# Kernel tuning notes

Hardware: AMD Instinct MI355X
Metric: run time of the kernel (lower is better)

## Reference

```python
import jax, jax.numpy as jnp
import numpy as np

D_MODEL = 1024
H = 16
D_HEAD = D_MODEL // H
MASK_VAL = -1e30


def setup_inputs() -> dict:
    key = jax.random.key(0)
    ks = jax.random.split(key, 10)
    B, S = 2, 2048
    scale = 1.0 / np.sqrt(D_MODEL)
    return {
        "query": jax.random.normal(ks[0], (B, S, D_MODEL), jnp.float32),
        "key": jax.random.normal(ks[1], (B, S, D_MODEL), jnp.float32),
        "value": jax.random.normal(ks[2], (B, S, D_MODEL), jnp.float32),
        "mask": jax.random.randint(ks[3], (B, S, S), 0, 2) > 0,
        "Wq": jax.random.normal(ks[4], (D_MODEL, D_MODEL), jnp.float32) * scale,
        "bq": jnp.zeros((D_MODEL,), jnp.float32),
        "Wk": jax.random.normal(ks[5], (D_MODEL, D_MODEL), jnp.float32) * scale,
        "bk": jnp.zeros((D_MODEL,), jnp.float32),
        "Wv": jax.random.normal(ks[6], (D_MODEL, D_MODEL), jnp.float32) * scale,
        "bv": jnp.zeros((D_MODEL,), jnp.float32),
    }


def _split_heads(x, B, S):
    # [B,S,D] -> [B,H,S,Dh]
    return x.reshape(B, S, H, D_HEAD).transpose(0, 2, 1, 3)


def reference(query, key, value, mask, Wq, bq, Wk, bk, Wv, bv):
    B, S, _ = query.shape
    q = _split_heads(query @ Wq.T + bq, B, S)
    k = _split_heads(key @ Wk.T + bk, B, S)
    v = _split_heads(value @ Wv.T + bv, B, S)
    # scale by sqrt of per-head dim (query.size(-1) after split)
    q = q / jnp.sqrt(jnp.asarray(D_HEAD, q.dtype))
    scores = jnp.einsum("bhqd,bhkd->bhqk", q, k)
    scores = jnp.where(mask[:, None, :, :], MASK_VAL, scores)
    attn = jax.nn.softmax(scores, axis=-1)
    out = jnp.einsum("bhqk,bhkd->bhqd", attn, v)
    return out.transpose(0, 2, 1, 3).reshape(B, S, D_MODEL)
```

## Files before the change

### kernel.cpp

```cpp
#include <hip/hip_runtime.h>
#include <hip/hip_bf16.h>

#define D_MODEL 1024
#define NH 16
#define DH 64
#define S_LEN 2048
#define BATCH 2
#define NEG_BIG -3e38f
#define QSCALE (0.125f * 1.44269504088896f)

#define KV_HSTRIDE (S_LEN * DH)
#define WS_V_OFF   (NH * KV_HSTRIDE)
#define KVB_WORDS  (2 * NH * KV_HSTRIDE)
#define MB_WORDS   ((S_LEN / 64) * S_LEN)
#define KTILE 128
#define NT (S_LEN / KTILE)
#define X_ELEMS (BATCH * S_LEN * D_MODEL)
#define W_ELEMS (D_MODEL * D_MODEL)
#define KSTR 88

typedef __attribute__((ext_vector_type(8))) short bf16x8;
typedef __attribute__((ext_vector_type(4))) float f32x4;

static __device__ inline unsigned short f2bf(float f) {
    union { float f; unsigned u; } v; v.f = f;
    unsigned r = v.u + 0x7fffu + ((v.u >> 16) & 1u);
    return (unsigned short)(r >> 16);
}
static __device__ inline unsigned cvt2(float a, float b) {
    union { __hip_bfloat162 h2; unsigned u; } cv;
    cv.h2 = __float22bfloat162_rn(make_float2(a, b));
    return cv.u;
}
static __device__ inline bf16x8 pack8(f32x4 a, f32x4 b) {
    union { bf16x8 v; unsigned u[4]; } r;
    r.u[0] = cvt2(a[0], a[1]); r.u[1] = cvt2(a[2], a[3]);
    r.u[2] = cvt2(b[0], b[1]); r.u[3] = cvt2(b[2], b[3]);
    return r.v;
}
static __device__ inline bf16x8 cvt8(const float* __restrict__ p) {
    return pack8(*(const f32x4*)p, *(const f32x4*)(p + 4));
}
static __device__ inline float exp2_fast(float x) {
#if __has_builtin(__builtin_amdgcn_exp2f)
    return __builtin_amdgcn_exp2f(x);
#else
    return exp2f(x);
#endif
}
static __device__ inline void gload_lds16(const unsigned short* __restrict__ g,
                                          unsigned short* l, int lane) {
#if __has_builtin(__builtin_amdgcn_global_load_lds)
    __builtin_amdgcn_global_load_lds(
        (const __attribute__((address_space(1))) void*)g,
        (__attribute__((address_space(3))) void*)l, 16, 0, 0);
#else
    *(bf16x8*)((char*)l + lane * 16) = *(const bf16x8*)g;
#endif
}
static __device__ inline int vperm(int s) {
    return (s & ~31) | ((s & 12) << 1) | ((s & 16) >> 2) | (s & 3);
}

__global__ __launch_bounds__(256) void cvt_kernel(
    const float* __restrict__ q, const float* __restrict__ k,
    const float* __restrict__ v,
    const float* __restrict__ Wq, const float* __restrict__ Wk,
    const float* __restrict__ Wv,
    unsigned short* __restrict__ xb, unsigned short* __restrict__ wb)
{
    const int by = blockIdx.y;
    const float* src;
    unsigned short* dst;
    int t;
    if (blockIdx.x < 1024) {
        src = by == 0 ? q : (by == 1 ? k : v);
        dst = xb + (size_t)by * X_ELEMS;
        t = blockIdx.x * 256 + threadIdx.x;
    } else {
        src = by == 0 ? Wq : (by == 1 ? Wk : Wv);
        dst = wb + (size_t)by * W_ELEMS;
        t = (blockIdx.x - 1024) * 256 + threadIdx.x;
    }
    const size_t o = (size_t)t * 16;
    *(bf16x8*)&dst[o]     = cvt8(src + o);
    *(bf16x8*)&dst[o + 8] = cvt8(src + o + 8);
}

__global__ __launch_bounds__(256) void pack_mask_kernel(
    const int* __restrict__ mask, unsigned long long* __restrict__ mbits,
    int b_base)
{
    const int w    = blockIdx.x * 4 + (threadIdx.x >> 6);
    const int lane = threadIdx.x & 63;
    const int b    = b_base + (w >> 16);
    const int rem  = w & 65535;
    const int kt   = rem >> 11;
    const int s    = rem & 2047;
    const int v = mask[((size_t)b * S_LEN + s) * S_LEN + kt * 64 + lane];
    const unsigned long long bits = __ballot(v != 0);
    if (lane == 0) mbits[w] = bits;
}

__global__ __launch_bounds__(256) void proj_v2_kernel(
    const unsigned short* __restrict__ xb, const unsigned short* __restrict__ wb,
    const float* __restrict__ bq, const float* __restrict__ bk,
    const float* __restrict__ bv,
    float* __restrict__ q_out, unsigned short* __restrict__ ws)
{
    const int bx = blockIdx.x;
    const int by = blockIdx.y;
    const int z  = by >> 3;
    const int c0 = (by & 7) * 128;

    const unsigned short* A  = xb + (size_t)z * X_ELEMS;
    const unsigned short* Bw = wb + (size_t)z * W_ELEMS;
    const float* bias = z == 0 ? bq : (z == 1 ? bk : bv);

    const int tid  = threadIdx.x;
    const int wave = tid >> 6;
    const int lane = tid & 63;
    const int quad = lane >> 4;
    const int l16  = lane & 15;
    const int m0   = (wave & 1) * 64;
    const int n0   = (wave >> 1) * 64;

    __shared__ __align__(16) unsigned short As[128 * 32];
    __shared__ __align__(16) unsigned short Bs[128 * 32];

    const int r_lo = wave * 16 + (lane >> 2);
    const int r_hi = (wave + 4) * 16 + (lane >> 2);
    const int segu = (lane & 3) * 8;
    const int row0 = bx * 128;

    f32x4 acc[4][4] = {};

    for (int kk = 0; kk < D_MODEL; kk += 32) {
        gload_lds16(A  + (size_t)(row0 + r_lo) * D_MODEL + kk + segu, &As[wave * 512], lane);
        gload_lds16(A  + (size_t)(row0 + r_hi) * D_MODEL + kk + segu, &As[(wave + 4) * 512], lane);
        gload_lds16(Bw + (size_t)(c0 + r_lo) * D_MODEL + kk + segu, &Bs[wave * 512], lane);
        gload_lds16(Bw + (size_t)(c0 + r_hi) * D_MODEL + kk + segu, &Bs[(wave + 4) * 512], lane);
        __syncthreads();

        bf16x8 af[4], bfr[4];
#pragma unroll
        for (int i = 0; i < 4; ++i)
            af[i] = *(const bf16x8*)&As[(m0 + i * 16 + l16) * 32 + quad * 8];
#pragma unroll
        for (int j = 0; j < 4; ++j)
            bfr[j] = *(const bf16x8*)&Bs[(n0 + j * 16 + l16) * 32 + quad * 8];
#pragma unroll
        for (int i = 0; i < 4; ++i)
#pragma unroll
            for (int j = 0; j < 4; ++j)
                acc[i][j] = __builtin_amdgcn_mfma_f32_16x16x32_bf16(
                    af[i], bfr[j], acc[i][j], 0, 0, 0);
        __syncthreads();
    }

#pragma unroll
    for (int j = 0; j < 4; ++j) {
        const int cl  = c0 + n0 + j * 16 + l16;
        const float bval = bias[cl];
        const int h  = cl >> 6;
        const int dh = cl & 63;
#pragma unroll
        for (int i = 0; i < 4; ++i) {
#pragma unroll
            for (int r = 0; r < 4; ++r) {
                const int row = row0 + m0 + i * 16 + quad * 4 + r;
                const float v = acc[i][j][r] + bval;
                if (z == 0) {
                    q_out[(size_t)row * D_MODEL + cl] = v * QSCALE;
                } else {
                    unsigned short* slab = ws + (size_t)(row >> 11) * KVB_WORDS;
                    const int s = row & 2047;
                    if (z == 1)
                        slab[(size_t)h * KV_HSTRIDE + s * DH + dh] = f2bf(v);
                    else
                        slab[WS_V_OFF + (size_t)h * KV_HSTRIDE + dh * S_LEN + vperm(s)] = f2bf(v);
                }
            }
        }
    }
}

__global__ __launch_bounds__(256) void proj_fb_kernel(
    const float* __restrict__ q_in, const float* __restrict__ k_in,
    const float* __restrict__ v_in,
    const float* __restrict__ Wq, const float* __restrict__ bq,
    const float* __restrict__ Wk, const float* __restrict__ bk,
    const float* __restrict__ Wv, const float* __restrict__ bv,
    float* __restrict__ q_out, unsigned short* __restrict__ ws, int b_base)
{
    const int bx = blockIdx.x;
    const int by = blockIdx.y;
    const int z  = by >> 3;
    const int c0 = (by & 7) * 128;

    const float* x    = z == 0 ? q_in : (z == 1 ? k_in : v_in);
    const float* W    = z == 0 ? Wq   : (z == 1 ? Wk   : Wv);
    const float* bias = z == 0 ? bq   : (z == 1 ? bk   : bv);

    const int tid  = threadIdx.x;
    const int wave = tid >> 6;
    const int lane = tid & 63;
    const int quad = lane >> 4;
    const int l16  = lane & 15;
    const int m0   = (wave & 1) * 64;
    const int n0   = (wave >> 1) * 64;

    __shared__ __align__(16) unsigned short As[128][40];
    __shared__ __align__(16) unsigned short Bs[128][40];

    const int srow = tid >> 1;
    const int kcol = (tid & 1) * 16;
    const int row0 = b_base * S_LEN + bx * 128;
    const float* ag = x + (size_t)(row0 + srow) * D_MODEL + kcol;
    const float* bg = W + (size_t)(c0 + srow) * D_MODEL + kcol;

    f32x4 acc[4][4] = {};

    for (int kk = 0; kk < D_MODEL; kk += 32) {
        {
            f32x4 a0 = *(const f32x4*)(ag + kk);
            f32x4 a1 = *(const f32x4*)(ag + kk + 4);
            f32x4 a2 = *(const f32x4*)(ag + kk + 8);
            f32x4 a3 = *(const f32x4*)(ag + kk + 12);
            f32x4 b0 = *(const f32x4*)(bg + kk);
            f32x4 b1 = *(const f32x4*)(bg + kk + 4);
            f32x4 b2 = *(const f32x4*)(bg + kk + 8);
            f32x4 b3 = *(const f32x4*)(bg + kk + 12);
            *(bf16x8*)&As[srow][kcol]     = pack8(a0, a1);
            *(bf16x8*)&As[srow][kcol + 8] = pack8(a2, a3);
            *(bf16x8*)&Bs[srow][kcol]     = pack8(b0, b1);
            *(bf16x8*)&Bs[srow][kcol + 8] = pack8(b2, b3);
        }
        __syncthreads();

        bf16x8 af[4], bfr[4];
#pragma unroll
        for (int i = 0; i < 4; ++i)
            af[i] = *(const bf16x8*)&As[m0 + i * 16 + l16][quad * 8];
#pragma unroll
        for (int j = 0; j < 4; ++j)
            bfr[j] = *(const bf16x8*)&Bs[n0 + j * 16 + l16][quad * 8];
#pragma unroll
        for (int i = 0; i < 4; ++i)
#pragma unroll
            for (int j = 0; j < 4; ++j)
                acc[i][j] = __builtin_amdgcn_mfma_f32_16x16x32_bf16(
                    af[i], bfr[j], acc[i][j], 0, 0, 0);
        __syncthreads();
    }

#pragma unroll
    for (int j = 0; j < 4; ++j) {
        const int cl  = c0 + n0 + j * 16 + l16;
        const float bval = bias[cl];
        const int h  = cl >> 6;
        const int dh = cl & 63;
#pragma unroll
        for (int i = 0; i < 4; ++i) {
#pragma unroll
            for (int r = 0; r < 4; ++r) {
                const int row = row0 + m0 + i * 16 + quad * 4 + r;
                const float v = acc[i][j][r] + bval;
                if (z == 0) {
                    q_out[(size_t)row * D_MODEL + cl] = v * QSCALE;
                } else {
                    const int b_rel = (row >> 11) - b_base;
                    const int s     = row & 2047;
                    unsigned short* slab = ws + (size_t)b_rel * KVB_WORDS;
                    if (z == 1)
                        slab[(size_t)h * KV_HSTRIDE + s * DH + dh] = f2bf(v);
                    else
                        slab[WS_V_OFF + (size_t)h * KV_HSTRIDE + dh * S_LEN + vperm(s)] = f2bf(v);
                }
            }
        }
    }
}

__global__ __launch_bounds__(256) void attn_kernel(
    const unsigned short* __restrict__ ws,
    const unsigned long long* __restrict__ mbits,
    const int* __restrict__ mask,
    float* __restrict__ out, int b_base, int use_bits)
{
    const int h     = blockIdx.x;
    const int qtile = blockIdx.y;
    const int bz    = blockIdx.z;
    const int b0    = b_base + bz;

    const unsigned short* K  = ws + (size_t)bz * KVB_WORDS + (size_t)h * KV_HSTRIDE;
    const unsigned short* Vg = K + WS_V_OFF;
    const unsigned long long* mb = mbits + (size_t)bz * MB_WORDS;

    const int tid  = threadIdx.x;
    const int wave = tid >> 6;
    const int lane = tid & 63;
    const int quad = lane >> 4;
    const int l16  = lane & 15;
    const int q0   = qtile * 64;

    __shared__ __align__(16) unsigned short Vt[64][136];
    __shared__ __align__(16) unsigned short Kt[128 * KSTR];

    bf16x8 aq0, aq1;
    {
        const float* qrow =
            out + (size_t)(b0 * S_LEN + q0 + wave * 16 + l16) * D_MODEL + h * DH;
        aq0 = cvt8(qrow + quad * 8);
        aq1 = cvt8(qrow + 32 + quad * 8);
    }

    const int qg = q0 + wave * 16 + l16;
    float l_lane = 0.f;
    f32x4 o_acc[4] = {};

    const int krow = tid >> 1, kc = (tid & 1) * 32;
    const int vrow = tid >> 2, vc = (tid & 3) * 32;
    bf16x8 kr[4], vr[4];
    {
        const unsigned short* kp = K + (size_t)krow * DH + kc;
        const unsigned short* vp = Vg + (size_t)vrow * S_LEN + vc;
#pragma unroll
        for (int i = 0; i < 4; ++i) {
            kr[i] = *(const bf16x8*)(kp + 8 * i);
            vr[i] = *(const bf16x8*)(vp + 8 * i);
        }
    }

    for (int kt = 0; kt < NT; ++kt) {
#pragma unroll
        for (int i = 0; i < 4; ++i) {
            *(bf16x8*)&Kt[krow * KSTR + kc + 8 * i] = kr[i];
            *(bf16x8*)&Vt[vrow][vc + 8 * i]         = vr[i];
        }
        __syncthreads();

        if (kt + 1 < NT) {
            const unsigned short* kp = K + (size_t)((kt + 1) * KTILE + krow) * DH + kc;
            const unsigned short* vp = Vg + (size_t)vrow * S_LEN + (kt + 1) * KTILE + vc;
#pragma unroll
            for (int i = 0; i < 4; ++i) {
                kr[i] = *(const bf16x8*)(kp + 8 * i);
                vr[i] = *(const bf16x8*)(vp + 8 * i);
            }
        }

        unsigned long long wm0 = 0ull, wm1 = 0ull;
        if (use_bits) {
            wm0 = mb[(size_t)(2 * kt) * S_LEN + qg] >> (quad * 4);
            wm1 = mb[(size_t)(2 * kt + 1) * S_LEN + qg] >> (quad * 4);
        }

        f32x4 s[8];
#pragma unroll
        for (int blk = 0; blk < 8; ++blk) {
            const unsigned short* kb = &Kt[(blk * 16 + l16) * KSTR];
            bf16x8 k0 = *(const bf16x8*)&kb[quad * 8];
            bf16x8 k1 = *(const bf16x8*)&kb[32 + quad * 8];
            s[blk] = (f32x4){0.f, 0.f, 0.f, 0.f};
            s[blk] = __builtin_amdgcn_mfma_f32_16x16x32_bf16(k0, aq0, s[blk], 0, 0, 0);
            s[blk] = __builtin_amdgcn_mfma_f32_16x16x32_bf16(k1, aq1, s[blk], 0, 0, 0);
        }

#pragma unroll
        for (int blk = 0; blk < 8; ++blk) {
            const unsigned long long w = (blk < 4) ? wm0 : wm1;
            const int sh = (blk & 3) * 16;
#pragma unroll
            for (int r = 0; r < 4; ++r) {
                bool masked;
                if (use_bits) {
                    masked = (w >> (sh + r)) & 1ull;
                } else {
                    const int kg = kt * KTILE + blk * 16 + quad * 4 + r;
                    masked = mask[((size_t)(b0 * S_LEN) + qg) * S_LEN + kg] != 0;
                }
                const float p = masked ? 0.0f : exp2_fast(s[blk][r]);
                s[blk][r] = p;
                l_lane += p;
            }
        }

        bf16x8 af[4];
#pragma unroll
        for (int c = 0; c < 4; ++c) {
            union { bf16x8 v; unsigned u[4]; } pk;
            pk.u[0] = cvt2(s[2 * c][0],     s[2 * c][1]);
            pk.u[1] = cvt2(s[2 * c][2],     s[2 * c][3]);
            pk.u[2] = cvt2(s[2 * c + 1][0], s[2 * c + 1][1]);
            pk.u[3] = cvt2(s[2 * c + 1][2], s[2 * c + 1][3]);
            af[c] = pk.v;
        }

#pragma unroll
        for (int d = 0; d < 4; ++d) {
#pragma unroll
            for (int c = 0; c < 4; ++c) {
                bf16x8 bv = *(const bf16x8*)&Vt[d * 16 + l16][c * 32 + quad * 8];
                o_acc[d] = __builtin_amdgcn_mfma_f32_16x16x32_bf16(af[c], bv, o_acc[d], 0, 0, 0);
            }
        }
        __syncthreads();
    }

    l_lane += __shfl_xor(l_lane, 16, 64);
    l_lane += __shfl_xor(l_lane, 32, 64);

#pragma unroll
    for (int r = 0; r < 4; ++r) {
        const float lsum = __shfl(l_lane, quad * 4 + r, 64);
        const float inv  = 1.0f / fmaxf(lsum, 1e-30f);
        const int qgr = q0 + wave * 16 + quad * 4 + r;
#pragma unroll
        for (int d = 0; d < 4; ++d)
            out[((size_t)(b0 * S_LEN) + qgr) * D_MODEL + h * DH + d * 16 + l16] =
                o_acc[d][r] * inv;
    }
}

extern "C" void kernel_launch(void* const* d_in, const int* in_sizes, int n_in,
                              void* d_out, int out_size, void* d_ws, size_t ws_size,
                              hipStream_t stream) {
    const float* query = (const float*)d_in[0];
    const float* key   = (const float*)d_in[1];
    const float* value = (const float*)d_in[2];
    const int*   mask  = (const int*)d_in[3];
    const float* Wq    = (const float*)d_in[4];
    const float* bq    = (const float*)d_in[5];
    const float* Wk    = (const float*)d_in[6];
    const float* bk    = (const float*)d_in[7];
    const float* Wv    = (const float*)d_in[8];
    const float* bv    = (const float*)d_in[9];

    unsigned short* ws   = (unsigned short*)d_ws;
    float*          outp = (float*)d_out;

    const size_t KV_BYTES = (size_t)KVB_WORDS * 2;
    const size_t MB_BYTES = (size_t)MB_WORDS * 8;
    const size_t XB_BYTES = (size_t)3 * X_ELEMS * 2;
    const size_t WB_BYTES = (size_t)3 * W_ELEMS * 2;
    const size_t base2    = 2 * KV_BYTES + 2 * MB_BYTES;

    if (ws_size >= base2 + XB_BYTES + WB_BYTES) {
        unsigned long long* mbits = (unsigned long long*)(ws + 2 * KVB_WORDS);
        unsigned short* xb = ws + base2 / 2;
        unsigned short* wb = xb + (size_t)3 * X_ELEMS;
        cvt_kernel<<<dim3(1280, 3), 256, 0, stream>>>(
            query, key, value, Wq, Wk, Wv, xb, wb);
        proj_v2_kernel<<<dim3(32, 24), 256, 0, stream>>>(
            xb, wb, bq, bk, bv, outp, ws);
        pack_mask_kernel<<<dim3(2 * MB_WORDS / 4), 256, 0, stream>>>(mask, mbits, 0);
        attn_kernel<<<dim3(NH, S_LEN / 64, 2), 256, 0, stream>>>(
            ws, mbits, mask, outp, 0, 1);
    } else if (ws_size >= base2) {
        unsigned long long* mbits = (unsigned long long*)(ws + 2 * KVB_WORDS);
        proj_fb_kernel<<<dim3(32, 24), 256, 0, stream>>>(
            query, key, value, Wq, bq, Wk, bk, Wv, bv, outp, ws, 0);
        pack_mask_kernel<<<dim3(2 * MB_WORDS / 4), 256, 0, stream>>>(mask, mbits, 0);
        attn_kernel<<<dim3(NH, S_LEN / 64, 2), 256, 0, stream>>>(
            ws, mbits, mask, outp, 0, 1);
    } else if (ws_size >= KV_BYTES + MB_BYTES) {
        unsigned long long* mbits = (unsigned long long*)(ws + KVB_WORDS);
        for (int b0 = 0; b0 < BATCH; ++b0) {
            proj_fb_kernel<<<dim3(16, 24), 256, 0, stream>>>(
                query, key, value, Wq, bq, Wk, bk, Wv, bv, outp, ws, b0);
            pack_mask_kernel<<<dim3(MB_WORDS / 4), 256, 0, stream>>>(mask, mbits, b0);
            attn_kernel<<<dim3(NH, S_LEN / 64, 1), 256, 0, stream>>>(
                ws, mbits, mask, outp, b0, 1);
        }
    } else {
        for (int b0 = 0; b0 < BATCH; ++b0) {
            proj_fb_kernel<<<dim3(16, 24), 256, 0, stream>>>(
                query, key, value, Wq, bq, Wk, bk, Wv, bv, outp, ws, b0);
            attn_kernel<<<dim3(NH, S_LEN / 64, 1), 256, 0, stream>>>(
                ws, (const unsigned long long*)ws, mask, outp, b0, 0);
        }
    }
}
```

Before: 274.4 us.

## Fuse mask packing into convert kernel, double K-step in projection, MFMA row sums

The f32-to-bf16 convert kernel and the mask bit-packing kernel now run as one flattened launch, which removes a kernel launch and lets the two memory-bound passes overlap. The projection GEMM loads two 32-wide K chunks per barrier pair, so it synchronises half as often at the cost of twice the LDS. The attention kernel computes softmax row sums with an extra MFMA against a ones vector, replacing per-element scalar adds and the final cross-lane shuffles. Because the sum now uses bf16-rounded probabilities, the normaliser matches the P·V product more closely but differs slightly from before.

```diff
diff --git a/kernel.cpp b/kernel.cpp
--- a/kernel.cpp
+++ b/kernel.cpp
@@ -6,7 +6,6 @@
 #define DH 64
 #define S_LEN 2048
 #define BATCH 2
-#define NEG_BIG -3e38f
 #define QSCALE (0.125f * 1.44269504088896f)
 
 #define KV_HSTRIDE (S_LEN * DH)
@@ -62,29 +61,50 @@
     return (s & ~31) | ((s & 12) << 1) | ((s & 16) >> 2) | (s & 3);
 }
 
-__global__ __launch_bounds__(256) void cvt_kernel(
+__global__ __launch_bounds__(256) void cvtpack_kernel(
     const float* __restrict__ q, const float* __restrict__ k,
     const float* __restrict__ v,
     const float* __restrict__ Wq, const float* __restrict__ Wk,
     const float* __restrict__ Wv,
-    unsigned short* __restrict__ xb, unsigned short* __restrict__ wb)
+    unsigned short* __restrict__ xb, unsigned short* __restrict__ wb,
+    const int* __restrict__ mask, unsigned long long* __restrict__ mbits)
 {
-    const int by = blockIdx.y;
-    const float* src;
-    unsigned short* dst;
-    int t;
-    if (blockIdx.x < 1024) {
-        src = by == 0 ? q : (by == 1 ? k : v);
-        dst = xb + (size_t)by * X_ELEMS;
-        t = blockIdx.x * 256 + threadIdx.x;
+    const int bid = blockIdx.x;
+    if (bid < 3840) {
+        const int z = bid / 1280;
+        const int r = bid - z * 1280;
+        const float* src;
+        unsigned short* dst;
+        int t;
+        if (r < 1024) {
+            src = z == 0 ? q : (z == 1 ? k : v);
+            dst = xb + (size_t)z * X_ELEMS;
+            t = r * 256 + threadIdx.x;
+        } else {
+            src = z == 0 ? Wq : (z == 1 ? Wk : Wv);
+            dst = wb + (size_t)z * W_ELEMS;
+            t = (r - 1024) * 256 + threadIdx.x;
+        }
+        const size_t o = (size_t)t * 16;
+        *(bf16x8*)&dst[o]     = cvt8(src + o);
+        *(bf16x8*)&dst[o + 8] = cvt8(src + o + 8);
     } else {
-        src = by == 0 ? Wq : (by == 1 ? Wk : Wv);
-        dst = wb + (size_t)by * W_ELEMS;
-        t = (blockIdx.x - 1024) * 256 + threadIdx.x;
-    }
-    const size_t o = (size_t)t * 16;
-    *(bf16x8*)&dst[o]     = cvt8(src + o);
-    *(bf16x8*)&dst[o + 8] = cvt8(src + o + 8);
+        const int pb   = bid - 3840;
+        const int wave = threadIdx.x >> 6;
+        const int lane = threadIdx.x & 63;
+        const int w0   = pb * 16 + wave * 4;
+#pragma unroll
+        for (int j = 0; j < 4; ++j) {
+            const int w   = w0 + j;
+            const int b   = w >> 16;
+            const int rem = w & 65535;
+            const int kt  = rem >> 11;
+            const int s   = rem & 2047;
+            const int vm  = mask[((size_t)b * S_LEN + s) * S_LEN + kt * 64 + lane];
+            const unsigned long long bits = __ballot(vm != 0);
+            if (lane == 0) mbits[w] = bits;
+        }
+    }
 }
 
 __global__ __launch_bounds__(256) void pack_mask_kernel(
@@ -125,8 +145,8 @@
     const int m0   = (wave & 1) * 64;
     const int n0   = (wave >> 1) * 64;
 
-    __shared__ __align__(16) unsigned short As[128 * 32];
-    __shared__ __align__(16) unsigned short Bs[128 * 32];
+    __shared__ __align__(16) unsigned short As[2][128 * 32];
+    __shared__ __align__(16) unsigned short Bs[2][128 * 32];
 
     const int r_lo = wave * 16 + (lane >> 2);
     const int r_hi = (wave + 4) * 16 + (lane >> 2);
@@ -135,26 +155,33 @@
 
     f32x4 acc[4][4] = {};
 
-    for (int kk = 0; kk < D_MODEL; kk += 32) {
-        gload_lds16(A  + (size_t)(row0 + r_lo) * D_MODEL + kk + segu, &As[wave * 512], lane);
-        gload_lds16(A  + (size_t)(row0 + r_hi) * D_MODEL + kk + segu, &As[(wave + 4) * 512], lane);
-        gload_lds16(Bw + (size_t)(c0 + r_lo) * D_MODEL + kk + segu, &Bs[wave * 512], lane);
-        gload_lds16(Bw + (size_t)(c0 + r_hi) * D_MODEL + kk + segu, &Bs[(wave + 4) * 512], lane);
+    for (int kk = 0; kk < D_MODEL; kk += 64) {
+#pragma unroll
+        for (int c = 0; c < 2; ++c) {
+            const int ko = kk + c * 32 + segu;
+            gload_lds16(A  + (size_t)(row0 + r_lo) * D_MODEL + ko, &As[c][wave * 512], lane);
+            gload_lds16(A  + (size_t)(row0 + r_hi) * D_MODEL + ko, &As[c][(wave + 4) * 512], lane);
+            gload_lds16(Bw + (size_t)(c0 + r_lo) * D_MODEL + ko, &Bs[c][wave * 512], lane);
+            gload_lds16(Bw + (size_t)(c0 + r_hi) * D_MODEL + ko, &Bs[c][(wave + 4) * 512], lane);
+        }
         __syncthreads();
 
-        bf16x8 af[4], bfr[4];
-#pragma unroll
-        for (int i = 0; i < 4; ++i)
-            af[i] = *(const bf16x8*)&As[(m0 + i * 16 + l16) * 32 + quad * 8];
-#pragma unroll
-        for (int j = 0; j < 4; ++j)
-            bfr[j] = *(const bf16x8*)&Bs[(n0 + j * 16 + l16) * 32 + quad * 8];
-#pragma unroll
-        for (int i = 0; i < 4; ++i)
+#pragma unroll
+        for (int c = 0; c < 2; ++c) {
+            bf16x8 af[4], bfr[4];
+#pragma unroll
+            for (int i = 0; i < 4; ++i)
+                af[i] = *(const bf16x8*)&As[c][(m0 + i * 16 + l16) * 32 + quad * 8];
 #pragma unroll
             for (int j = 0; j < 4; ++j)
-                acc[i][j] = __builtin_amdgcn_mfma_f32_16x16x32_bf16(
-                    af[i], bfr[j], acc[i][j], 0, 0, 0);
+                bfr[j] = *(const bf16x8*)&Bs[c][(n0 + j * 16 + l16) * 32 + quad * 8];
+#pragma unroll
+            for (int i = 0; i < 4; ++i)
+#pragma unroll
+                for (int j = 0; j < 4; ++j)
+                    acc[i][j] = __builtin_amdgcn_mfma_f32_16x16x32_bf16(
+                        af[i], bfr[j], acc[i][j], 0, 0, 0);
+        }
         __syncthreads();
     }
 
@@ -315,8 +342,16 @@
         aq1 = cvt8(qrow + 32 + quad * 8);
     }
 
+    bf16x8 ones;
+    {
+        union { bf16x8 v; unsigned short u[8]; } o;
+#pragma unroll
+        for (int i = 0; i < 8; ++i) o.u[i] = 0x3F80;
+        ones = o.v;
+    }
+
     const int qg = q0 + wave * 16 + l16;
-    float l_lane = 0.f;
+    f32x4 l_acc = {0.f, 0.f, 0.f, 0.f};
     f32x4 o_acc[4] = {};
 
     const int krow = tid >> 1, kc = (tid & 1) * 32;
@@ -380,9 +415,7 @@
                     const int kg = kt * KTILE + blk * 16 + quad * 4 + r;
                     masked = mask[((size_t)(b0 * S_LEN) + qg) * S_LEN + kg] != 0;
                 }
-                const float p = masked ? 0.0f : exp2_fast(s[blk][r]);
-                s[blk][r] = p;
-                l_lane += p;
+                s[blk][r] = masked ? 0.0f : exp2_fast(s[blk][r]);
             }
         }
 
@@ -398,6 +431,10 @@
         }
 
 #pragma unroll
+        for (int c = 0; c < 4; ++c)
+            l_acc = __builtin_amdgcn_mfma_f32_16x16x32_bf16(af[c], ones, l_acc, 0, 0, 0);
+
+#pragma unroll
         for (int d = 0; d < 4; ++d) {
 #pragma unroll
             for (int c = 0; c < 4; ++c) {
@@ -408,13 +445,9 @@
         __syncthreads();
     }
 
-    l_lane += __shfl_xor(l_lane, 16, 64);
-    l_lane += __shfl_xor(l_lane, 32, 64);
-
 #pragma unroll
     for (int r = 0; r < 4; ++r) {
-        const float lsum = __shfl(l_lane, quad * 4 + r, 64);
-        const float inv  = 1.0f / fmaxf(lsum, 1e-30f);
+        const float inv = 1.0f / fmaxf(l_acc[r], 1e-30f);
         const int qgr = q0 + wave * 16 + quad * 4 + r;
 #pragma unroll
         for (int d = 0; d < 4; ++d)
@@ -450,11 +483,10 @@
         unsigned long long* mbits = (unsigned long long*)(ws + 2 * KVB_WORDS);
         unsigned short* xb = ws + base2 / 2;
         unsigned short* wb = xb + (size_t)3 * X_ELEMS;
-        cvt_kernel<<<dim3(1280, 3), 256, 0, stream>>>(
-            query, key, value, Wq, Wk, Wv, xb, wb);
+        cvtpack_kernel<<<dim3(3840 + 8192), 256, 0, stream>>>(
+            query, key, value, Wq, Wk, Wv, xb, wb, mask, mbits);
         proj_v2_kernel<<<dim3(32, 24), 256, 0, stream>>>(
             xb, wb, bq, bk, bv, outp, ws);
-        pack_mask_kernel<<<dim3(2 * MB_WORDS / 4), 256, 0, stream>>>(mask, mbits, 0);
         attn_kernel<<<dim3(NH, S_LEN / 64, 2), 256, 0, stream>>>(
             ws, mbits, mask, outp, 0, 1);
     } else if (ws_size >= base2) {
```

Measured after the change: 284.7 us. 3.8% more time.
